# Kernel tuning notes

Hardware: AMD Instinct MI355X
Metric: run time of the kernel (lower is better)

The kernel has to match this reference:

```python
import jax, jax.numpy as jnp
import numpy as np
import math

B, S, D = 2, 2048, 1024
H, DH = 16, 64          # n_heads, d_head = d_model // n_heads
WINDOW = 256            # window_size


def setup_inputs() -> dict:
    key = jax.random.key(0)
    ks = jax.random.split(key, 9)
    scale = 0.02
    return {
        "x":  jax.random.normal(ks[0], (B, S, D), dtype=jnp.float32),
        "wq": jax.random.normal(ks[1], (D, D), dtype=jnp.float32) * scale,
        "bq": jnp.zeros((D,), dtype=jnp.float32),
        "wk": jax.random.normal(ks[2], (D, D), dtype=jnp.float32) * scale,
        "bk": jnp.zeros((D,), dtype=jnp.float32),
        "wv": jax.random.normal(ks[3], (D, D), dtype=jnp.float32) * scale,
        "bv": jnp.zeros((D,), dtype=jnp.float32),
        "wo": jax.random.normal(ks[4], (D, D), dtype=jnp.float32) * scale,
        "bo": jnp.zeros((D,), dtype=jnp.float32),
    }


def reference(x, wq, bq, wk, bk, wv, bv, wo, bo):
    b, s, d = x.shape
    # QKV projections -> [b, h, s, dh]
    q = (x @ wq + bq).reshape(b, s, H, DH).transpose(0, 2, 1, 3)
    k = (x @ wk + bk).reshape(b, s, H, DH).transpose(0, 2, 1, 3)
    v = (x @ wv + bv).reshape(b, s, H, DH).transpose(0, 2, 1, 3)

    scores = jnp.einsum("bhqd,bhkd->bhqk", q, k) / math.sqrt(DH)

    # causal + local-window mask: j <= i and i - j <= window
    idx = jnp.arange(s)
    row = idx[:, None]
    col = idx[None, :]
    mask = (col <= row) & (row - col <= WINDOW)        # [s, s]
    scores = jnp.where(mask[None, None, :, :], scores, -jnp.inf)

    attn = jax.nn.softmax(scores, axis=-1)
    # torch.nan_to_num(attn, 0.0): rows always include the diagonal so no NaNs,
    # but keep faithful behavior.
    attn = jnp.nan_to_num(attn, nan=0.0)

    out = jnp.einsum("bhqk,bhkd->bhqd", attn, v)        # [b, h, s, dh]
    out = out.transpose(0, 2, 1, 3).reshape(b, s, d)
    return out @ wo + bo
```

## Files before the change

kernel.cpp:

```cpp
#include <hip/hip_runtime.h>

#define B_ 2
#define S_ 2048
#define D_ 1024
#define H_ 16
#define DH_ 64
#define WIN_ 256
#define VTS 2080

typedef __attribute__((ext_vector_type(8))) short bf16x8;
typedef __attribute__((ext_vector_type(4))) float f32x4;
typedef unsigned short u16;

#define MFMA(a, b, c) __builtin_amdgcn_mfma_f32_16x16x32_bf16((a), (b), (c), 0, 0, 0)

__device__ __forceinline__ u16 f2b(float f) {
  unsigned int u = __float_as_uint(f);
  u += 0x7fffu + ((u >> 16) & 1u);
  return (u16)(u >> 16);
}

__device__ __forceinline__ float b2f(u16 b) {
  return __uint_as_float(((unsigned int)b) << 16);
}

__device__ __forceinline__ unsigned int pkbf(float lo, float hi) {
  unsigned int r;
  asm("v_cvt_pk_bf16_f32 %0, %1, %2" : "=v"(r) : "v"(lo), "v"(hi));
  return r;
}

__device__ __forceinline__ void async_cp16(const void* g, void* l) {
  __builtin_amdgcn_global_load_lds(
      (const __attribute__((address_space(1))) void*)g,
      (__attribute__((address_space(3))) void*)l, 16, 0, 0);
}

__global__ void k_prep(const float* __restrict__ x,
                       const float* __restrict__ wq, const float* __restrict__ wk,
                       const float* __restrict__ wv, const float* __restrict__ wo,
                       u16* __restrict__ xb, u16* __restrict__ wqkvt, u16* __restrict__ wot) {
  __shared__ float tile[64][65];
  const int bx = blockIdx.x;
  const int t = threadIdx.x;
  if (bx < 1024) {
    const int t0 = (bx * 256 + t) * 4;
#pragma unroll
    for (int it = 0; it < 4; it++) {
      int i = t0 + it * 1048576;
      float4 v = *(const float4*)(x + i);
      ushort4 o;
      o.x = f2b(v.x); o.y = f2b(v.y); o.z = f2b(v.z); o.w = f2b(v.w);
      *(ushort4*)(xb + i) = o;
    }
    return;
  }
  const int tb = bx - 1024;
  const int z = tb >> 8, rest = tb & 255;
  const float* W = z == 0 ? wq : z == 1 ? wk : z == 2 ? wv : wo;
  u16* T = z < 3 ? wqkvt + (size_t)z * 1024 * 1024 : wot;
  const int bn = (rest & 15) * 64;
  const int bk = (rest >> 4) * 64;
  const int r = t >> 4;
  const int c = (t & 15) * 4;
#pragma unroll
  for (int i = 0; i < 4; i++) {
    float4 v = *(const float4*)(W + (size_t)(bk + r + i * 16) * D_ + bn + c);
    tile[c + 0][r + i * 16] = v.x;
    tile[c + 1][r + i * 16] = v.y;
    tile[c + 2][r + i * 16] = v.z;
    tile[c + 3][r + i * 16] = v.w;
  }
  __syncthreads();
  const int n = t >> 2, seg = (t & 3) * 16;
  __align__(16) u16 tmp[16];
#pragma unroll
  for (int u = 0; u < 16; u++) tmp[u] = f2b(tile[n][seg + u]);
  uint4* dst = (uint4*)(T + (size_t)(bn + n) * D_ + bk + seg);
  dst[0] = ((uint4*)tmp)[0];
  dst[1] = ((uint4*)tmp)[1];
}

__device__ __forceinline__ void gemm_core128(const u16* __restrict__ Ag, const u16* __restrict__ Btg,
                                             u16* As, u16* Bs, f32x4 (&acc)[4][4],
                                             int m0, int n0) {
  const int tid = threadIdx.x;
  const int w = tid >> 6, lane = tid & 63;
  const int quad = lane >> 4, l15 = lane & 15;
  const int wm = (w & 1) * 64, wn = (w >> 1) * 64;
  const int rowa = tid >> 3;
  const int colsw = (((tid & 7) ^ (rowa & 7)) * 8);
  const u16* ap = Ag + (size_t)(m0 + rowa) * D_ + colsw;
  const u16* bp = Btg + (size_t)(n0 + rowa) * D_ + colsw;
  u16* As0 = As + w * 512;
  u16* Bs0 = Bs + w * 512;
  const int c0 = ((quad * 8) ^ ((l15 & 7) * 8));
  for (int kb = 0; kb < D_; kb += 64) {
#pragma unroll
    for (int i = 0; i < 4; i++) {
      async_cp16(ap + kb + (size_t)(i * 32) * D_, As0 + i * 2048);
      async_cp16(bp + kb + (size_t)(i * 32) * D_, Bs0 + i * 2048);
    }
    __syncthreads();
#pragma unroll
    for (int kh = 0; kh < 2; kh++) {
      const int c = c0 ^ (kh * 32);
      bf16x8 af[4], bfr[4];
#pragma unroll
      for (int i = 0; i < 4; i++) af[i] = *(const bf16x8*)&As[(wm + i * 16 + l15) * 64 + c];
#pragma unroll
      for (int j = 0; j < 4; j++) bfr[j] = *(const bf16x8*)&Bs[(wn + j * 16 + l15) * 64 + c];
#pragma unroll
      for (int i = 0; i < 4; i++)
#pragma unroll
        for (int j = 0; j < 4; j++) acc[i][j] = MFMA(af[i], bfr[j], acc[i][j]);
    }
    __syncthreads();
  }
}

__global__ __launch_bounds__(256, 3) void k_gemm_qkv(
    const u16* __restrict__ xb, const u16* __restrict__ wqkvt,
    const float* __restrict__ bq, const float* __restrict__ bk_, const float* __restrict__ bv,
    u16* __restrict__ Qg, u16* __restrict__ Kg, u16* __restrict__ Vt) {
  __shared__ __align__(16) u16 smem[17408];
  u16* As = smem;
  u16* Bs = smem + 8192;
  const int L = blockIdx.x;
  const int xcd = L & 7, slot = L >> 3;
  const int mblk = (xcd >> 1) * 8 + (slot & 7);
  const int nblk = (xcd & 1) * 12 + (slot >> 3);
  const int n0 = nblk * 128, m0 = mblk * 128;
  const int z = n0 >> 10;
  const float* bias = z == 0 ? bq : z == 1 ? bk_ : bv;
  f32x4 acc[4][4] = {};
  gemm_core128(xb, wqkvt, As, Bs, acc, m0, n0);

  const int tid = threadIdx.x;
  const int w = tid >> 6, lane = tid & 63;
  const int quad = lane >> 4, l15 = lane & 15;
  const int wm = (w & 1) * 64, wn = (w >> 1) * 64;
  const int nloc = n0 & 1023;
  float biasv[4];
#pragma unroll
  for (int j = 0; j < 4; j++) biasv[j] = bias[nloc + wn + j * 16 + l15];
  const int b_ = m0 >> 11, sb = m0 & 2047;
  const float scale = z == 0 ? 0.125f * 1.44269504f : 1.0f;
  const int row = tid >> 4, ch = tid & 15;

  if (z < 2) {
#pragma unroll
    for (int j = 0; j < 4; j++)
#pragma unroll
      for (int i = 0; i < 4; i++)
#pragma unroll
        for (int r = 0; r < 4; r++)
          smem[(wm + i * 16 + quad * 4 + r) * 136 + wn + j * 16 + l15] =
              f2b((acc[i][j][r] + biasv[j]) * scale);
    __syncthreads();
    u16* OG = z == 0 ? Qg : Kg;
#pragma unroll
    for (int it = 0; it < 8; it++) {
      int rr = row + it * 16;
      bf16x8 v = *(const bf16x8*)&smem[rr * 136 + ch * 8];
      *(bf16x8*)(OG + (size_t)(m0 + rr) * D_ + nloc + ch * 8) = v;
    }
  } else {
#pragma unroll
    for (int j = 0; j < 4; j++)
#pragma unroll
      for (int i = 0; i < 4; i++)
#pragma unroll
        for (int r = 0; r < 4; r++)
          smem[(wn + j * 16 + l15) * 136 + wm + i * 16 + quad * 4 + r] =
              f2b(acc[i][j][r] + biasv[j]);
    __syncthreads();
#pragma unroll
    for (int it = 0; it < 8; it++) {
      int nn = nloc + row + it * 16;
      int h = nn >> 6, dh = nn & 63;
      bf16x8 v = *(const bf16x8*)&smem[(row + it * 16) * 136 + ch * 8];
      *(bf16x8*)(Vt + ((size_t)(b_ * H_ + h) * DH_ + dh) * VTS + sb + ch * 8) = v;
    }
  }
}

__global__ __launch_bounds__(256, 2) void k_gemm_out(
    const u16* __restrict__ Ab, const u16* __restrict__ wot,
    const float* __restrict__ bo, float* __restrict__ out) {
  __shared__ __align__(16) u16 smem[24576];
  u16* As = smem;
  u16* Bs = smem + 8192;
  const int L = blockIdx.x;
  const int xcd = L & 7, slot = L >> 3;
  const int mblk = xcd * 8 + (slot & 7);
  const int nblk = slot >> 3;
  const int n0 = nblk * 128, m0 = mblk * 64;
  const int tid = threadIdx.x;
  const int w = tid >> 6, lane = tid & 63;
  const int quad = lane >> 4, l15 = lane & 15;
  const int wn = w * 32;
  const int rowa = tid >> 4;
  const int gg = (tid & 15) ^ rowa;
  const u16* ap = Ab + (size_t)(m0 + rowa) * D_ + gg * 8;
  const u16* bp = wot + (size_t)(n0 + rowa) * D_ + gg * 8;
  u16* As0 = As + w * 512;
  u16* Bs0 = Bs + w * 512;
  f32x4 acc[4][2] = {};
  for (int kb = 0; kb < D_; kb += 128) {
#pragma unroll
    for (int i = 0; i < 4; i++)
      async_cp16(ap + kb + (size_t)(i * 16) * D_, As0 + i * 2048);
#pragma unroll
    for (int i = 0; i < 8; i++)
      async_cp16(bp + kb + (size_t)(i * 16) * D_, Bs0 + i * 2048);
    __syncthreads();
#pragma unroll
    for (int kh = 0; kh < 4; kh++) {
      const int cs = (((quad + 4 * kh) ^ l15) * 8);
      bf16x8 af[4], bfr[2];
#pragma unroll
      for (int i = 0; i < 4; i++) af[i] = *(const bf16x8*)&As[(i * 16 + l15) * 128 + cs];
#pragma unroll
      for (int j = 0; j < 2; j++) bfr[j] = *(const bf16x8*)&Bs[(wn + j * 16 + l15) * 128 + cs];
#pragma unroll
      for (int i = 0; i < 4; i++)
#pragma unroll
        for (int j = 0; j < 2; j++) acc[i][j] = MFMA(af[i], bfr[j], acc[i][j]);
    }
    __syncthreads();
  }
  float biasv[2];
#pragma unroll
  for (int j = 0; j < 2; j++) biasv[j] = bo[n0 + wn + j * 16 + l15];
#pragma unroll
  for (int j = 0; j < 2; j++)
#pragma unroll
    for (int i = 0; i < 4; i++)
#pragma unroll
      for (int r = 0; r < 4; r++)
        smem[(i * 16 + quad * 4 + r) * 136 + wn + j * 16 + l15] = f2b(acc[i][j][r] + biasv[j]);
  __syncthreads();
  const int row = tid >> 4, ch = tid & 15;
#pragma unroll
  for (int it = 0; it < 4; it++) {
    int rr = row + it * 16;
    bf16x8 v = *(const bf16x8*)&smem[rr * 136 + ch * 8];
    float4 f0, f1;
    f0.x = b2f((u16)v[0]); f0.y = b2f((u16)v[1]); f0.z = b2f((u16)v[2]); f0.w = b2f((u16)v[3]);
    f1.x = b2f((u16)v[4]); f1.y = b2f((u16)v[5]); f1.z = b2f((u16)v[6]); f1.w = b2f((u16)v[7]);
    float* dst = out + (size_t)(m0 + rr) * D_ + n0 + ch * 8;
    *(float4*)dst = f0;
    *(float4*)(dst + 4) = f1;
  }
}

__global__ __launch_bounds__(256, 2) void k_attn(
    const u16* __restrict__ Qg, const u16* __restrict__ Kg,
    const u16* __restrict__ Vt, u16* __restrict__ Ab) {
  __shared__ __align__(16) u16 Plds[4][32 * 72];
  const int tid = threadIdx.x;
  const int w = tid >> 6, lane = tid & 63;
  const int quad = lane >> 4, l15 = lane & 15;
  const int lid = blockIdx.x;
  const int xcd = lid & 7, slot = lid >> 3;
  const int bh = xcd * 4 + (slot & 3);
  const int qb = slot >> 2;
  const int qw = qb * 128 + w * 32;
  const int b_ = bh >> 4, h = bh & 15;

  const u16* QbaseA = Qg + (size_t)(b_ * S_ + qw + l15) * D_ + h * DH_ + quad * 8;
  bf16x8 aq0 = *(const bf16x8*)QbaseA;
  bf16x8 aq1 = *(const bf16x8*)(QbaseA + 32);
  const u16* QbaseB = QbaseA + (size_t)16 * D_;
  bf16x8 bq0 = *(const bf16x8*)QbaseB;
  bf16x8 bq1 = *(const bf16x8*)(QbaseB + 32);

  float lrA = 0.f, lrB = 0.f;
  f32x4 OA[4] = {}, OB[4] = {};

  const u16* Kb = Kg + (size_t)b_ * S_ * D_ + h * DH_ + quad * 8;
  const u16* Vb = Vt + (size_t)bh * DH_ * VTS + (size_t)l15 * VTS + quad * 8;
  const int klo = qw >= WIN_ ? qw - WIN_ : 0;
  const int qA = qw + l15, qB = qA + 16;
  const int qwB = qw + 16;
  const int srcA = l15 + ((quad & 1) ? 32 : 0);
  const int srcB = srcA + 16;

  bf16x8 k00, k01, k10, k11, v0, v1, v2, v3;
  {
    const u16* Kt0 = Kb + (size_t)(klo + l15) * D_;
    k00 = *(const bf16x8*)Kt0;
    k01 = *(const bf16x8*)(Kt0 + 32);
    k10 = *(const bf16x8*)(Kt0 + (size_t)16 * D_);
    k11 = *(const bf16x8*)(Kt0 + (size_t)16 * D_ + 32);
    const u16* Vt0 = Vb + klo;
    v0 = *(const bf16x8*)(Vt0);
    v1 = *(const bf16x8*)(Vt0 + (size_t)16 * VTS);
    v2 = *(const bf16x8*)(Vt0 + (size_t)32 * VTS);
    v3 = *(const bf16x8*)(Vt0 + (size_t)48 * VTS);
  }

  for (int k0 = klo;;) {
    const int kn = k0 + 32;
    const bool more = kn <= qw;
    bf16x8 nk00, nk01, nk10, nk11, nv0, nv1, nv2, nv3;
    if (more) {
      const u16* Kt0 = Kb + (size_t)(kn + l15) * D_;
      nk00 = *(const bf16x8*)Kt0;
      nk01 = *(const bf16x8*)(Kt0 + 32);
      nk10 = *(const bf16x8*)(Kt0 + (size_t)16 * D_);
      nk11 = *(const bf16x8*)(Kt0 + (size_t)16 * D_ + 32);
      const u16* Vt0 = Vb + kn;
      nv0 = *(const bf16x8*)(Vt0);
      nv1 = *(const bf16x8*)(Vt0 + (size_t)16 * VTS);
      nv2 = *(const bf16x8*)(Vt0 + (size_t)32 * VTS);
      nv3 = *(const bf16x8*)(Vt0 + (size_t)48 * VTS);
    }

    const bool computeA = (k0 <= qw + 15);
    const bool computeB = (k0 + 31 >= qwB - WIN_);

    if (computeA) {
      f32x4 s0 = {0.f, 0.f, 0.f, 0.f}, s1 = {0.f, 0.f, 0.f, 0.f};
      __builtin_amdgcn_s_setprio(1);
      s0 = MFMA(k00, aq0, s0);
      s0 = MFMA(k01, aq1, s0);
      s1 = MFMA(k10, aq0, s1);
      s1 = MFMA(k11, aq1, s1);
      __builtin_amdgcn_s_setprio(0);
      const bool interior = (k0 >= qw + 15 - WIN_) && (k0 + 31 <= qw);
      float e[8];
      if (interior) {
#pragma unroll
        for (int r = 0; r < 4; r++) {
          float p0 = __builtin_amdgcn_exp2f(s0[r]);
          float p1 = __builtin_amdgcn_exp2f(s1[r]);
          e[r] = p0; e[4 + r] = p1;
          lrA += p0 + p1;
        }
      } else {
#pragma unroll
        for (int r = 0; r < 4; r++) {
          int key0 = k0 + quad * 4 + r;
          int key1 = key0 + 16;
          float p0 = (key0 <= qA && key0 + WIN_ >= qA) ? __builtin_amdgcn_exp2f(s0[r]) : 0.f;
          float p1 = (key1 <= qA && key1 + WIN_ >= qA) ? __builtin_amdgcn_exp2f(s1[r]) : 0.f;
          e[r] = p0; e[4 + r] = p1;
          lrA += p0 + p1;
        }
      }
      unsigned int s0p01 = pkbf(e[0], e[1]);
      unsigned int s0p23 = pkbf(e[2], e[3]);
      unsigned int s1p01 = pkbf(e[4], e[5]);
      unsigned int s1p23 = pkbf(e[6], e[7]);
      unsigned int a0 = (unsigned)__shfl((int)s0p01, srcA);
      unsigned int a1 = (unsigned)__shfl((int)s0p23, srcA);
      unsigned int a2 = (unsigned)__shfl((int)s0p01, srcB);
      unsigned int a3 = (unsigned)__shfl((int)s0p23, srcB);
      unsigned int c0 = (unsigned)__shfl((int)s1p01, srcA);
      unsigned int c1 = (unsigned)__shfl((int)s1p23, srcA);
      unsigned int c2 = (unsigned)__shfl((int)s1p01, srcB);
      unsigned int c3 = (unsigned)__shfl((int)s1p23, srcB);
      union { unsigned int u[4]; bf16x8 v; } pf;
      const bool lo = quad < 2;
      pf.u[0] = lo ? a0 : c0;
      pf.u[1] = lo ? a1 : c1;
      pf.u[2] = lo ? a2 : c2;
      pf.u[3] = lo ? a3 : c3;
      __builtin_amdgcn_s_setprio(1);
      OA[0] = MFMA(v0, pf.v, OA[0]);
      OA[1] = MFMA(v1, pf.v, OA[1]);
      OA[2] = MFMA(v2, pf.v, OA[2]);
      OA[3] = MFMA(v3, pf.v, OA[3]);
      __builtin_amdgcn_s_setprio(0);
    }

    if (computeB) {
      f32x4 s0 = {0.f, 0.f, 0.f, 0.f}, s1 = {0.f, 0.f, 0.f, 0.f};
      __builtin_amdgcn_s_setprio(1);
      s0 = MFMA(k00, bq0, s0);
      s0 = MFMA(k01, bq1, s0);
      s1 = MFMA(k10, bq0, s1);
      s1 = MFMA(k11, bq1, s1);
      __builtin_amdgcn_s_setprio(0);
      const bool interior = (k0 >= qwB + 15 - WIN_) && (k0 + 31 <= qwB);
      float e[8];
      if (interior) {
#pragma unroll
        for (int r = 0; r < 4; r++) {
          float p0 = __builtin_amdgcn_exp2f(s0[r]);
          float p1 = __builtin_amdgcn_exp2f(s1[r]);
          e[r] = p0; e[4 + r] = p1;
          lrB += p0 + p1;
        }
      } else {
#pragma unroll
        for (int r = 0; r < 4; r++) {
          int key0 = k0 + quad * 4 + r;
          int key1 = key0 + 16;
          float p0 = (key0 <= qB && key0 + WIN_ >= qB) ? __builtin_amdgcn_exp2f(s0[r]) : 0.f;
          float p1 = (key1 <= qB && key1 + WIN_ >= qB) ? __builtin_amdgcn_exp2f(s1[r]) : 0.f;
          e[r] = p0; e[4 + r] = p1;
          lrB += p0 + p1;
        }
      }
      unsigned int s0p01 = pkbf(e[0], e[1]);
      unsigned int s0p23 = pkbf(e[2], e[3]);
      unsigned int s1p01 = pkbf(e[4], e[5]);
      unsigned int s1p23 = pkbf(e[6], e[7]);
      unsigned int a0 = (unsigned)__shfl((int)s0p01, srcA);
      unsigned int a1 = (unsigned)__shfl((int)s0p23, srcA);
      unsigned int a2 = (unsigned)__shfl((int)s0p01, srcB);
      unsigned int a3 = (unsigned)__shfl((int)s0p23, srcB);
      unsigned int c0 = (unsigned)__shfl((int)s1p01, srcA);
      unsigned int c1 = (unsigned)__shfl((int)s1p23, srcA);
      unsigned int c2 = (unsigned)__shfl((int)s1p01, srcB);
      unsigned int c3 = (unsigned)__shfl((int)s1p23, srcB);
      union { unsigned int u[4]; bf16x8 v; } pf;
      const bool lo = quad < 2;
      pf.u[0] = lo ? a0 : c0;
      pf.u[1] = lo ? a1 : c1;
      pf.u[2] = lo ? a2 : c2;
      pf.u[3] = lo ? a3 : c3;
      __builtin_amdgcn_s_setprio(1);
      OB[0] = MFMA(v0, pf.v, OB[0]);
      OB[1] = MFMA(v1, pf.v, OB[1]);
      OB[2] = MFMA(v2, pf.v, OB[2]);
      OB[3] = MFMA(v3, pf.v, OB[3]);
      __builtin_amdgcn_s_setprio(0);
    }

    if (!more) break;
    k00 = nk00; k01 = nk01; k10 = nk10; k11 = nk11;
    v0 = nv0; v1 = nv1; v2 = nv2; v3 = nv3;
    k0 = kn;
  }

  lrA += __shfl_xor(lrA, 16);
  lrA += __shfl_xor(lrA, 32);
  lrB += __shfl_xor(lrB, 16);
  lrB += __shfl_xor(lrB, 32);
  const float invA = 1.0f / lrA;
  const float invB = 1.0f / lrB;

  u16* P = &Plds[w][0];
#pragma unroll
  for (int j = 0; j < 4; j++)
#pragma unroll
    for (int r = 0; r < 4; r++) {
      P[l15 * 72 + j * 16 + quad * 4 + r] = f2b(OA[j][r] * invA);
      P[(l15 + 16) * 72 + j * 16 + quad * 4 + r] = f2b(OB[j][r] * invB);
    }
#pragma unroll
  for (int it = 0; it < 2; it++) {
    int rq = (lane >> 2) + it * 16, cc = lane & 3;
    bf16x8 ov0 = *(const bf16x8*)&P[rq * 72 + cc * 16];
    bf16x8 ov1 = *(const bf16x8*)&P[rq * 72 + cc * 16 + 8];
    u16* dst = Ab + (size_t)(b_ * S_ + qw + rq) * D_ + h * DH_ + cc * 16;
    *(bf16x8*)dst = ov0;
    *(bf16x8*)(dst + 8) = ov1;
  }
}

extern "C" void kernel_launch(void* const* d_in, const int* in_sizes, int n_in,
                              void* d_out, int out_size, void* d_ws, size_t ws_size,
                              hipStream_t stream) {
  const float* x  = (const float*)d_in[0];
  const float* wq = (const float*)d_in[1];
  const float* bq = (const float*)d_in[2];
  const float* wk = (const float*)d_in[3];
  const float* bk = (const float*)d_in[4];
  const float* wv = (const float*)d_in[5];
  const float* bv = (const float*)d_in[6];
  const float* wo = (const float*)d_in[7];
  const float* bo = (const float*)d_in[8];

  char* ws = (char*)d_ws;
  const size_t MB = 1u << 20;
  u16* Qg    = (u16*)(ws + 0 * MB);
  u16* Kg    = (u16*)(ws + 8 * MB);
  u16* Vt    = (u16*)(ws + 16 * MB);
  u16* Ab    = (u16*)(ws + 25 * MB);
  u16* xb    = (u16*)(ws + 33 * MB);
  u16* wqkvt = (u16*)(ws + 41 * MB);
  u16* wot   = (u16*)(ws + 47 * MB);

  k_prep<<<2048, 256, 0, stream>>>(x, wq, wk, wv, wo, xb, wqkvt, wot);
  k_gemm_qkv<<<768, 256, 0, stream>>>(xb, wqkvt, bq, bk, bv, Qg, Kg, Vt);
  k_attn<<<512, 256, 0, stream>>>(Qg, Kg, Vt, Ab);
  k_gemm_out<<<512, 256, 0, stream>>>(Ab, wot, bo, (float*)d_out);
}
```

Before: 153.6 us.

## Double-buffer QKV GEMM shared-memory tiles with async prefetch

Inlines the QKV GEMM main loop and splits shared memory into two stages. The next K-tile's async global-to-LDS copies are issued before computing on the current tile, with a partial vmcnt wait and raw barriers, so load latency overlaps MFMA work. Doubling LDS to 64KB lowers the launch-bounds occupancy hint from 3 to 2 blocks per CU. The risk is lower occupancy and correctness depending on the vmcnt count matching the number of outstanding copies.

```diff
diff --git a/kernel.cpp b/kernel.cpp
--- a/kernel.cpp
+++ b/kernel.cpp
@@ -81,51 +81,11 @@
   dst[1] = ((uint4*)tmp)[1];
 }
 
-__device__ __forceinline__ void gemm_core128(const u16* __restrict__ Ag, const u16* __restrict__ Btg,
-                                             u16* As, u16* Bs, f32x4 (&acc)[4][4],
-                                             int m0, int n0) {
-  const int tid = threadIdx.x;
-  const int w = tid >> 6, lane = tid & 63;
-  const int quad = lane >> 4, l15 = lane & 15;
-  const int wm = (w & 1) * 64, wn = (w >> 1) * 64;
-  const int rowa = tid >> 3;
-  const int colsw = (((tid & 7) ^ (rowa & 7)) * 8);
-  const u16* ap = Ag + (size_t)(m0 + rowa) * D_ + colsw;
-  const u16* bp = Btg + (size_t)(n0 + rowa) * D_ + colsw;
-  u16* As0 = As + w * 512;
-  u16* Bs0 = Bs + w * 512;
-  const int c0 = ((quad * 8) ^ ((l15 & 7) * 8));
-  for (int kb = 0; kb < D_; kb += 64) {
-#pragma unroll
-    for (int i = 0; i < 4; i++) {
-      async_cp16(ap + kb + (size_t)(i * 32) * D_, As0 + i * 2048);
-      async_cp16(bp + kb + (size_t)(i * 32) * D_, Bs0 + i * 2048);
-    }
-    __syncthreads();
-#pragma unroll
-    for (int kh = 0; kh < 2; kh++) {
-      const int c = c0 ^ (kh * 32);
-      bf16x8 af[4], bfr[4];
-#pragma unroll
-      for (int i = 0; i < 4; i++) af[i] = *(const bf16x8*)&As[(wm + i * 16 + l15) * 64 + c];
-#pragma unroll
-      for (int j = 0; j < 4; j++) bfr[j] = *(const bf16x8*)&Bs[(wn + j * 16 + l15) * 64 + c];
-#pragma unroll
-      for (int i = 0; i < 4; i++)
-#pragma unroll
-        for (int j = 0; j < 4; j++) acc[i][j] = MFMA(af[i], bfr[j], acc[i][j]);
-    }
-    __syncthreads();
-  }
-}
-
-__global__ __launch_bounds__(256, 3) void k_gemm_qkv(
+__global__ __launch_bounds__(256, 2) void k_gemm_qkv(
     const u16* __restrict__ xb, const u16* __restrict__ wqkvt,
     const float* __restrict__ bq, const float* __restrict__ bk_, const float* __restrict__ bv,
     u16* __restrict__ Qg, u16* __restrict__ Kg, u16* __restrict__ Vt) {
-  __shared__ __align__(16) u16 smem[17408];
-  u16* As = smem;
-  u16* Bs = smem + 8192;
+  __shared__ __align__(16) u16 smem[32768];
   const int L = blockIdx.x;
   const int xcd = L & 7, slot = L >> 3;
   const int mblk = (xcd >> 1) * 8 + (slot & 7);
@@ -133,13 +93,64 @@
   const int n0 = nblk * 128, m0 = mblk * 128;
   const int z = n0 >> 10;
   const float* bias = z == 0 ? bq : z == 1 ? bk_ : bv;
-  f32x4 acc[4][4] = {};
-  gemm_core128(xb, wqkvt, As, Bs, acc, m0, n0);
 
   const int tid = threadIdx.x;
   const int w = tid >> 6, lane = tid & 63;
   const int quad = lane >> 4, l15 = lane & 15;
   const int wm = (w & 1) * 64, wn = (w >> 1) * 64;
+  const int rowa = tid >> 3;
+  const int colsw = (((tid & 7) ^ (rowa & 7)) * 8);
+  const u16* ap = xb + (size_t)(m0 + rowa) * D_ + colsw;
+  const u16* bp = wqkvt + (size_t)(n0 + rowa) * D_ + colsw;
+  const int c0 = ((quad * 8) ^ ((l15 & 7) * 8));
+  f32x4 acc[4][4] = {};
+
+#define STAGE(kb, buf)                                                            \
+  {                                                                               \
+    u16* As0 = smem + (buf)*16384 + w * 512;                                      \
+    u16* Bs0 = smem + (buf)*16384 + 8192 + w * 512;                               \
+    _Pragma("unroll")                                                             \
+    for (int i = 0; i < 4; i++) {                                                 \
+      async_cp16(ap + (kb) + (size_t)(i * 32) * D_, As0 + i * 2048);              \
+      async_cp16(bp + (kb) + (size_t)(i * 32) * D_, Bs0 + i * 2048);              \
+    }                                                                             \
+  }
+
+#define COMPUTE(buf)                                                              \
+  {                                                                               \
+    const u16* As = smem + (buf)*16384;                                           \
+    const u16* Bs = smem + (buf)*16384 + 8192;                                    \
+    _Pragma("unroll")                                                             \
+    for (int kh = 0; kh < 2; kh++) {                                              \
+      const int c = c0 ^ (kh * 32);                                               \
+      bf16x8 af[4], bfr[4];                                                       \
+      _Pragma("unroll")                                                           \
+      for (int i = 0; i < 4; i++) af[i] = *(const bf16x8*)&As[(wm + i * 16 + l15) * 64 + c]; \
+      _Pragma("unroll")                                                           \
+      for (int j = 0; j < 4; j++) bfr[j] = *(const bf16x8*)&Bs[(wn + j * 16 + l15) * 64 + c]; \
+      _Pragma("unroll")                                                           \
+      for (int i = 0; i < 4; i++)                                                 \
+        _Pragma("unroll")                                                         \
+        for (int j = 0; j < 4; j++) acc[i][j] = MFMA(af[i], bfr[j], acc[i][j]);   \
+    }                                                                             \
+  }
+
+  STAGE(0, 0);
+  for (int t = 0; t < 15; ++t) {
+    const int cur = t & 1;
+    STAGE((t + 1) * 64, cur ^ 1);
+    asm volatile("s_waitcnt vmcnt(8)" ::: "memory");
+    __builtin_amdgcn_s_barrier();
+    COMPUTE(cur);
+    __builtin_amdgcn_s_barrier();
+  }
+  asm volatile("s_waitcnt vmcnt(0)" ::: "memory");
+  __builtin_amdgcn_s_barrier();
+  COMPUTE(1);
+  __syncthreads();
+#undef STAGE
+#undef COMPUTE
+
   const int nloc = n0 & 1023;
   float biasv[4];
 #pragma unroll
```

New measurement: 153.2 us. Within noise of the previous version (-0.3%).
